# Kernel tuning notes

Hardware: AMD Instinct MI355X
Metric: run time of the kernel (lower is better)

The kernel has to match this reference:

```python
import jax, jax.numpy as jnp
import numpy as np

B, T, D, H = 64, 512, 512, 1024
IMG = 2048

def setup_inputs() -> dict:
    key = jax.random.key(0)
    ks = jax.random.split(key, 8)
    s_ih = 1.0 / np.sqrt(H)
    return {
        "x": jax.random.normal(ks[0], (B, T, D), dtype=jnp.float32),
        "img_context": jax.random.normal(ks[1], (B, IMG), dtype=jnp.float32),
        "W_ih": jax.random.uniform(ks[2], (4 * H, D), dtype=jnp.float32, minval=-s_ih, maxval=s_ih),
        "W_hh": jax.random.uniform(ks[3], (4 * H, H), dtype=jnp.float32, minval=-s_ih, maxval=s_ih),
        "b_ih": jax.random.uniform(ks[4], (4 * H,), dtype=jnp.float32, minval=-s_ih, maxval=s_ih),
        "b_hh": jax.random.uniform(ks[5], (4 * H,), dtype=jnp.float32, minval=-s_ih, maxval=s_ih),
        "W_m": jax.random.uniform(ks[6], (H, IMG), dtype=jnp.float32, minval=-1.0/np.sqrt(IMG), maxval=1.0/np.sqrt(IMG)),
    }

def reference(x, img_context, W_ih, W_hh, b_ih, b_hh, W_m):
    hid = W_hh.shape[1]
    # Multimodal gate d = M(img_context); loop-invariant, hoisted out of the scan.
    d = img_context @ W_m.T  # [B, H]
    # Precompute input projections for all timesteps in one GEMM: [T, B, 4H]
    xs = jnp.transpose(x, (1, 0, 2))  # [T, B, D]
    x_proj = jnp.einsum('tbd,gd->tbg', xs, W_ih) + b_ih + b_hh

    def step(carry, xp):
        h, c = carry
        h = h * d  # multimodal gating multiply applied before the cell
        gates = xp + h @ W_hh.T  # [B, 4H]
        i, f, g, o = jnp.split(gates, 4, axis=-1)
        i = jax.nn.sigmoid(i)
        f = jax.nn.sigmoid(f)
        g = jnp.tanh(g)
        o = jax.nn.sigmoid(o)
        c = f * c + i * g
        h = o * jnp.tanh(c)
        return (h, c), h

    h0 = jnp.zeros((x.shape[0], hid), dtype=x.dtype)
    c0 = jnp.zeros((x.shape[0], hid), dtype=x.dtype)
    (hn, cn), outs = jax.lax.scan(step, (h0, c0), x_proj)
    out = jnp.transpose(outs, (1, 0, 2))  # [B, T, H]
    return out, hn, cn
```

## Files before the change

kernel.cpp:

```cpp
#include <hip/hip_runtime.h>
#include <math.h>

constexpr int B_   = 64;
constexpr int T_   = 512;
constexpr int D_   = 512;
constexpr int H_   = 1024;
constexpr int IMG_ = 2048;
constexpr int NWG  = 256;
constexpr int NTHR = 256;

constexpr size_t SLOT_U16   = (size_t)B_ * H_;
constexpr size_t RING_BYTES = (size_t)(T_ + 1) * SLOT_U16 * 2;
constexpr size_t XBF_BYTES  = (size_t)B_ * T_ * D_ * 2;
constexpr unsigned SENT32   = 0x7F7F7F7Fu;

typedef __attribute__((ext_vector_type(8))) short    short8;
typedef __attribute__((ext_vector_type(4))) float    f32x4;
typedef __attribute__((ext_vector_type(4))) unsigned uint4v;

__device__ __forceinline__ unsigned short f2bf(float f) {
  unsigned u = __float_as_uint(f);
  u += 0x7FFFu + ((u >> 16) & 1u);
  return (unsigned short)(u >> 16);
}
__device__ __forceinline__ float sigf(float v) {
  return __fdividef(1.0f, 1.0f + __expf(-v));
}
__device__ __forceinline__ float tanhfast(float v) {
  v = fminf(15.0f, fmaxf(-15.0f, v));
  const float e = __expf(2.0f * v);
  return __fdividef(e - 1.0f, e + 1.0f);
}
__device__ __forceinline__ short8 pk8(const float4 a, const float4 b) {
  union { unsigned u[4]; short8 s; } r;
  asm("v_cvt_pk_bf16_f32 %0, %1, %2" : "=v"(r.u[0]) : "v"(a.x), "v"(a.y));
  asm("v_cvt_pk_bf16_f32 %0, %1, %2" : "=v"(r.u[1]) : "v"(a.z), "v"(a.w));
  asm("v_cvt_pk_bf16_f32 %0, %1, %2" : "=v"(r.u[2]) : "v"(b.x), "v"(b.y));
  asm("v_cvt_pk_bf16_f32 %0, %1, %2" : "=v"(r.u[3]) : "v"(b.z), "v"(b.w));
  return r.s;
}

__global__ void __launch_bounds__(NTHR)
x_repack_kernel(const float* __restrict__ x, unsigned short* __restrict__ x_bf) {
  const int idx = blockIdx.x * NTHR + threadIdx.x;
  const int k8 = idx & 63;
  const int t  = (idx >> 6) & 511;
  const int b  = idx >> 15;
  const float* px = x + ((size_t)b * T_ + t) * D_ + k8 * 8;
  const float4 v0 = *(const float4*)px;
  const float4 v1 = *(const float4*)(px + 4);
  const size_t off = ((size_t)(t * 4 + (b >> 4)) * 16 + (k8 >> 2)) * 512
                   + (size_t)(k8 & 3) * 128 + (size_t)(b & 15) * 8;
  *(short8*)(x_bf + off) = pk8(v0, v1);
}

template<int RING, int XBF>
__global__ void __launch_bounds__(NTHR, 1)
mmlstm_persistent(const float* __restrict__ x,
                  const unsigned short* __restrict__ x_bf,
                  const float* __restrict__ img,
                  const float* __restrict__ W_ih,
                  const float* __restrict__ W_hh,
                  const float* __restrict__ b_ih,
                  const float* __restrict__ b_hh,
                  const float* __restrict__ W_m,
                  float* __restrict__ out,
                  float* __restrict__ hn,
                  float* __restrict__ cn,
                  unsigned* __restrict__ flags,
                  unsigned short* __restrict__ ring)
{
  __shared__ float gaccs[4][16][68];
  __shared__ float bias_lds[64];
  __shared__ char  ldspad[72 * 1024];

  const int tid  = threadIdx.x;
  const int lane = tid & 63;
  const int wv   = tid >> 6;
  const int wg   = blockIdx.x;
  const int q    = wg & 3;
  const int cgid = wg >> 2;
  const int b0   = q * 16;
  const int j0   = cgid * 16;

  ((volatile char*)ldspad)[tid] = 0;

  unsigned* myflags = flags + q * 64;
  unsigned* myslot  = myflags + cgid;

  const int cloc = lane & 15;
  const int ko8  = (lane >> 4) << 3;
  short8 wx[4][4], wh[4][8];
  #pragma unroll
  for (int tile = 0; tile < 4; ++tile) {
    const int grow = tile * H_ + j0 + cloc;
    #pragma unroll
    for (int sx = 0; sx < 4; ++sx) {
      const float* p = W_ih + (size_t)grow * D_ + (wv + 4 * sx) * 32 + ko8;
      wx[tile][sx] = pk8(*(const float4*)p, *(const float4*)(p + 4));
    }
    #pragma unroll
    for (int sh = 0; sh < 8; ++sh) {
      const float* p = W_hh + (size_t)grow * H_ + (wv + 4 * sh) * 32 + ko8;
      wh[tile][sh] = pk8(*(const float4*)p, *(const float4*)(p + 4));
    }
  }
  if (tid < 64) {
    const int grow = (tid >> 4) * H_ + j0 + (tid & 15);
    bias_lds[tid] = b_ih[grow] + b_hh[grow];
  }

  const int b_l = tid >> 4;
  const int jj  = tid & 15;
  const int b   = b0 + b_l;
  const int j   = j0 + jj;

  const int poff = (j >> 5) * 512 + ((j >> 3) & 3) * 128 + b_l * 8 + (j & 7);

  float dval = 0.0f;
  {
    const float4* ir = (const float4*)(img + (size_t)b * IMG_);
    const float4* wr = (const float4*)(W_m + (size_t)j * IMG_);
    for (int k = 0; k < IMG_ / 4; ++k) {
      const float4 a = ir[k];
      const float4 w = wr[k];
      dval += a.x * w.x + a.y * w.y + a.z * w.z + a.w * w.w;
    }
  }

  if ((jj & 1) == 0)
    __hip_atomic_store((unsigned*)(ring + (size_t)q * 16384 + poff), 0u,
                       __ATOMIC_RELAXED, __HIP_MEMORY_SCOPE_AGENT);

  float cstate = 0.0f;

  __syncthreads();
  if (RING == 0 && tid == 0)
    __hip_atomic_store(myslot, 1u, __ATOMIC_RELAXED, __HIP_MEMORY_SCOPE_AGENT);

  auto pollFlags = [&](unsigned target) {
    for (;;) {
      const unsigned f = __hip_atomic_load(myflags + lane, __ATOMIC_RELAXED,
                                           __HIP_MEMORY_SCOPE_AGENT);
      if (__all(f >= target)) break;
    }
  };

  short8 xr[4];
  auto xprefetch = [&](int t) {
    if (XBF) {
      const unsigned short* xb = x_bf + ((size_t)t * 4 + q) * 8192;
      #pragma unroll
      for (int sx = 0; sx < 4; ++sx)
        xr[sx] = *(const short8*)(xb + (size_t)(wv + 4 * sx) * 512 + lane * 8);
    } else {
      const float* rb = x + ((size_t)(b0 + cloc) * T_ + t) * D_ + ko8;
      #pragma unroll
      for (int sx = 0; sx < 4; ++sx) {
        const float* p = rb + (wv + 4 * sx) * 32;
        xr[sx] = pk8(*(const float4*)p, *(const float4*)(p + 4));
      }
    }
  };

  xprefetch(0);

  for (int t = 0; t < T_; ++t) {
    const unsigned short* sp = ring + (size_t)(RING ? t : (t & 1)) * SLOT_U16
                             + (size_t)q * 16384;
    short8 hfr[8];
    if (RING) {
      for (;;) {
        uint4v tmp[8];
        #pragma unroll
        for (int sh = 0; sh < 8; ++sh) {
          const unsigned short* ap = sp + (size_t)(wv + 4 * sh) * 512 + lane * 8;
          asm volatile("global_load_dwordx4 %0, %1, off sc0 sc1"
                       : "=&v"(tmp[sh]) : "v"(ap));
        }
        asm volatile("s_waitcnt vmcnt(0)" ::: "memory");
        __builtin_amdgcn_sched_barrier(0);
        bool ok = true;
        #pragma unroll
        for (int sh = 0; sh < 8; ++sh)
          #pragma unroll
          for (int e = 0; e < 4; ++e)
            ok &= (tmp[sh][e] != SENT32);
        if (__all(ok)) {
          #pragma unroll
          for (int sh = 0; sh < 8; ++sh) hfr[sh] = *(short8*)&tmp[sh];
          break;
        }
      }
    } else {
      pollFlags((unsigned)(t + 1));
      asm volatile("" ::: "memory");
      uint4v tmp[8];
      #pragma unroll
      for (int sh = 0; sh < 8; ++sh) {
        const unsigned short* ap = sp + (size_t)(wv + 4 * sh) * 512 + lane * 8;
        asm volatile("global_load_dwordx4 %0, %1, off sc0 sc1" : "=&v"(tmp[sh]) : "v"(ap));
      }
      asm volatile("s_waitcnt vmcnt(0)" ::: "memory");
      __builtin_amdgcn_sched_barrier(0);
      #pragma unroll
      for (int sh = 0; sh < 8; ++sh)
        hfr[sh] = *(short8*)&tmp[sh];
    }

    f32x4 ac[4];
    #pragma unroll
    for (int tile = 0; tile < 4; ++tile) ac[tile] = (f32x4){0.f, 0.f, 0.f, 0.f};
    #pragma unroll
    for (int sx = 0; sx < 4; ++sx) {
      #pragma unroll
      for (int tile = 0; tile < 4; ++tile)
        ac[tile] = __builtin_amdgcn_mfma_f32_16x16x32_bf16(xr[sx], wx[tile][sx], ac[tile], 0, 0, 0);
    }
    #pragma unroll
    for (int sh = 0; sh < 8; ++sh) {
      #pragma unroll
      for (int tile = 0; tile < 4; ++tile)
        ac[tile] = __builtin_amdgcn_mfma_f32_16x16x32_bf16(hfr[sh], wh[tile][sh], ac[tile], 0, 0, 0);
    }

    {
      const int crow = (lane >> 4) * 4;
      #pragma unroll
      for (int tile = 0; tile < 4; ++tile) {
        #pragma unroll
        for (int rr = 0; rr < 4; ++rr)
          gaccs[wv][crow + rr][tile * 16 + cloc] = ac[tile][rr];
      }
    }
    asm volatile("s_waitcnt lgkmcnt(0)" ::: "memory");
    __builtin_amdgcn_s_barrier();
    __builtin_amdgcn_sched_barrier(0);

    float gv[4];
    #pragma unroll
    for (int g = 0; g < 4; ++g) {
      const int c = g * 16 + jj;
      gv[g] = gaccs[0][b_l][c] + gaccs[1][b_l][c] + gaccs[2][b_l][c] + gaccs[3][b_l][c]
            + bias_lds[c];
    }
    const float ig = sigf(gv[0]);
    const float fg = sigf(gv[1]);
    const float gg = tanhfast(gv[2]);
    const float og = sigf(gv[3]);
    cstate = fg * cstate + ig * gg;
    const float h = og * tanhfast(cstate);

    {
      const unsigned hd  = f2bf(h * dval);
      const unsigned nxt = __shfl_down((int)hd, 1);
      if ((jj & 1) == 0)
        __hip_atomic_store((unsigned*)(ring + (size_t)(RING ? (t + 1) : ((t + 1) & 1)) * SLOT_U16
                                       + (size_t)q * 16384 + poff),
                           hd | (nxt << 16),
                           __ATOMIC_RELAXED, __HIP_MEMORY_SCOPE_AGENT);
    }

    if (RING) {
      __builtin_amdgcn_s_barrier();
      __builtin_amdgcn_sched_barrier(0);
    } else {
      __syncthreads();
      if (t < T_ - 1 && tid == 0)
        __hip_atomic_store(myslot, (unsigned)(t + 2), __ATOMIC_RELAXED, __HIP_MEMORY_SCOPE_AGENT);
    }

    __builtin_nontemporal_store(h, &out[((size_t)b * T_ + t) * H_ + j]);
    if (t == T_ - 1) {
      hn[(size_t)b * H_ + j] = h;
      cn[(size_t)b * H_ + j] = cstate;
    } else {
      xprefetch(t + 1);
    }
  }
}

extern "C" void kernel_launch(void* const* d_in, const int* in_sizes, int n_in,
                              void* d_out, int out_size, void* d_ws, size_t ws_size,
                              hipStream_t stream) {
  (void)in_sizes; (void)n_in; (void)out_size;
  const float* x    = (const float*)d_in[0];
  const float* img  = (const float*)d_in[1];
  const float* W_ih = (const float*)d_in[2];
  const float* W_hh = (const float*)d_in[3];
  const float* b_ih = (const float*)d_in[4];
  const float* b_hh = (const float*)d_in[5];
  const float* W_m  = (const float*)d_in[6];

  float* out = (float*)d_out;
  float* hn  = out + (size_t)B_ * T_ * H_;
  float* cn  = hn + (size_t)B_ * H_;

  unsigned*       flags = (unsigned*)d_ws;
  unsigned short* ring  = (unsigned short*)((char*)d_ws + 4096);
  unsigned short* x_bf  = (unsigned short*)((char*)d_ws + 4096 + RING_BYTES);

  hipMemsetAsync(d_ws, 0, 4096, stream);

  if (ws_size >= 4096 + RING_BYTES + XBF_BYTES) {
    hipMemsetAsync(ring, 0x7F, RING_BYTES, stream);
    hipLaunchKernelGGL(x_repack_kernel, dim3((B_ * T_ * D_ / 8) / NTHR), dim3(NTHR), 0, stream,
                       x, x_bf);
    hipLaunchKernelGGL((mmlstm_persistent<1, 1>), dim3(NWG), dim3(NTHR), 0, stream,
                       x, x_bf, img, W_ih, W_hh, b_ih, b_hh, W_m, out, hn, cn, flags, ring);
  } else if (ws_size >= 4096 + RING_BYTES) {
    hipMemsetAsync(ring, 0x7F, RING_BYTES, stream);
    hipLaunchKernelGGL((mmlstm_persistent<1, 0>), dim3(NWG), dim3(NTHR), 0, stream,
                       x, x_bf, img, W_ih, W_hh, b_ih, b_hh, W_m, out, hn, cn, flags, ring);
  } else {
    hipLaunchKernelGGL((mmlstm_persistent<0, 0>), dim3(NWG), dim3(NTHR), 0, stream,
                       x, x_bf, img, W_ih, W_hh, b_ih, b_hh, W_m, out, hn, cn, flags, ring);
  }
}
```

Baseline: 1.324 ms.

## Double-buffer gate LDS to drop per-step barrier and poll only stale ring chunks

Gate accumulator LDS is double-buffered by timestep parity, which lets the ring path drop its second workgroup barrier per step. The spin on the h ring now re-polls only the 8 chunks still holding sentinels instead of reloading all of them. Both aim to shorten the serial per-step critical path of the persistent LSTM. The padding LDS is shrunk to make room for the larger buffer, which keeps the 1-block-per-CU occupancy intent.

```diff
diff --git a/kernel.cpp b/kernel.cpp
--- a/kernel.cpp
+++ b/kernel.cpp
@@ -70,9 +70,9 @@
                   unsigned* __restrict__ flags,
                   unsigned short* __restrict__ ring)
 {
-  __shared__ float gaccs[4][16][68];
+  __shared__ float gaccs[2][4][16][68];
   __shared__ float bias_lds[64];
-  __shared__ char  ldspad[72 * 1024];
+  __shared__ char  ldspad[52 * 1024];
 
   const int tid  = threadIdx.x;
   const int lane = tid & 63;
@@ -170,28 +170,46 @@
                              + (size_t)q * 16384;
     short8 hfr[8];
     if (RING) {
-      for (;;) {
-        uint4v tmp[8];
+      uint4v tmp[8];
+      #pragma unroll
+      for (int sh = 0; sh < 8; ++sh) {
+        const unsigned short* ap = sp + (size_t)(wv + 4 * sh) * 512 + lane * 8;
+        asm volatile("global_load_dwordx4 %0, %1, off sc0 sc1"
+                     : "=&v"(tmp[sh]) : "v"(ap));
+      }
+      asm volatile("s_waitcnt vmcnt(0)" ::: "memory");
+      __builtin_amdgcn_sched_barrier(0);
+      unsigned pend = 0;
+      #pragma unroll
+      for (int sh = 0; sh < 8; ++sh) {
+        bool ok = true;
+        #pragma unroll
+        for (int e = 0; e < 4; ++e) ok &= (tmp[sh][e] != SENT32);
+        if (!__all(ok)) pend |= (1u << sh);
+      }
+      while (pend) {
         #pragma unroll
         for (int sh = 0; sh < 8; ++sh) {
-          const unsigned short* ap = sp + (size_t)(wv + 4 * sh) * 512 + lane * 8;
-          asm volatile("global_load_dwordx4 %0, %1, off sc0 sc1"
-                       : "=&v"(tmp[sh]) : "v"(ap));
+          if (pend & (1u << sh)) {
+            const unsigned short* ap = sp + (size_t)(wv + 4 * sh) * 512 + lane * 8;
+            asm volatile("global_load_dwordx4 %0, %1, off sc0 sc1"
+                         : "=&v"(tmp[sh]) : "v"(ap));
+          }
         }
         asm volatile("s_waitcnt vmcnt(0)" ::: "memory");
         __builtin_amdgcn_sched_barrier(0);
-        bool ok = true;
         #pragma unroll
-        for (int sh = 0; sh < 8; ++sh)
-          #pragma unroll
-          for (int e = 0; e < 4; ++e)
-            ok &= (tmp[sh][e] != SENT32);
-        if (__all(ok)) {
-          #pragma unroll
-          for (int sh = 0; sh < 8; ++sh) hfr[sh] = *(short8*)&tmp[sh];
-          break;
+        for (int sh = 0; sh < 8; ++sh) {
+          if (pend & (1u << sh)) {
+            bool ok = true;
+            #pragma unroll
+            for (int e = 0; e < 4; ++e) ok &= (tmp[sh][e] != SENT32);
+            if (__all(ok)) pend &= ~(1u << sh);
+          }
         }
       }
+      #pragma unroll
+      for (int sh = 0; sh < 8; ++sh) hfr[sh] = *(short8*)&tmp[sh];
     } else {
       pollFlags((unsigned)(t + 1));
       asm volatile("" ::: "memory");
@@ -230,7 +248,7 @@
       for (int tile = 0; tile < 4; ++tile) {
         #pragma unroll
         for (int rr = 0; rr < 4; ++rr)
-          gaccs[wv][crow + rr][tile * 16 + cloc] = ac[tile][rr];
+          gaccs[t & 1][wv][crow + rr][tile * 16 + cloc] = ac[tile][rr];
       }
     }
     asm volatile("s_waitcnt lgkmcnt(0)" ::: "memory");
@@ -241,7 +259,8 @@
     #pragma unroll
     for (int g = 0; g < 4; ++g) {
       const int c = g * 16 + jj;
-      gv[g] = gaccs[0][b_l][c] + gaccs[1][b_l][c] + gaccs[2][b_l][c] + gaccs[3][b_l][c]
+      gv[g] = gaccs[t & 1][0][b_l][c] + gaccs[t & 1][1][b_l][c]
+            + gaccs[t & 1][2][b_l][c] + gaccs[t & 1][3][b_l][c]
             + bias_lds[c];
     }
     const float ig = sigf(gv[0]);
@@ -261,10 +280,7 @@
                            __ATOMIC_RELAXED, __HIP_MEMORY_SCOPE_AGENT);
     }
 
-    if (RING) {
-      __builtin_amdgcn_s_barrier();
-      __builtin_amdgcn_sched_barrier(0);
-    } else {
+    if (RING == 0) {
       __syncthreads();
       if (t < T_ - 1 && tid == 0)
         __hip_atomic_store(myslot, (unsigned)(t + 2), __ATOMIC_RELAXED, __HIP_MEMORY_SCOPE_AGENT);
```

After: 1.282 ms (median of 3 runs). 1.03x faster.
